# Optimization experiments

Hardware: AMD Instinct MI355X
Metric: run time of the kernel (lower is better)

The kernel has to match this reference:

```python
import jax, jax.numpy as jnp
import numpy as np

PAST = 15        # sum(num_classes[:-1])
NC = 20          # sum(num_classes)
ALPHA = 0.99
IGNORE = 255


def setup_inputs() -> dict:
    key = jax.random.key(0)
    k1, k2, k3, k4, k5, k6 = jax.random.split(key, 6)
    B, C, H, W = 8, NC, 512, 512
    logit = jax.random.normal(k1, (B, C, H, W), dtype=jnp.float32)
    # ema_prob is used as probabilities (gathered & compared to thresholds)
    ema_prob = jax.nn.softmax(jax.random.normal(k2, (B, C, H, W), dtype=jnp.float32), axis=1)
    ema_thresh = jax.random.uniform(k3, (NC,), dtype=jnp.float32, minval=0.2, maxval=0.8)
    real_labels = jax.random.randint(k4, (B, H, W), 0, NC, dtype=jnp.int64)
    # sprinkle ignore pixels (255) like real segmentation masks
    real_labels = jnp.where(jax.random.uniform(k5, (B, H, W)) < 0.1, IGNORE, real_labels)
    moving_prob_avg = jax.random.uniform(k6, (NC,), dtype=jnp.float32)
    return {"logit": logit, "ema_prob": ema_prob, "ema_thresh": ema_thresh,
            "real_labels": real_labels, "moving_prob_avg": moving_prob_avg}


def reference(logit, ema_prob, ema_thresh, real_labels, moving_prob_avg):
    # --- pseudo-labels from current model (detached softmax) ---
    logit_prob = jax.nn.softmax(jax.lax.stop_gradient(logit), axis=1)  # [B,C,H,W]
    labels = jnp.argmax(logit_prob[:, :PAST], axis=1)                   # [B,H,W]
    labels = jnp.where(real_labels >= PAST, real_labels, labels)
    idx = jnp.where(real_labels == IGNORE, 0, labels)
    scores = jnp.take_along_axis(logit_prob, idx[:, None], axis=1)[:, 0]  # [B,H,W]

    # --- per-class mean of scores + EMA update of moving_prob_avg ---
    flat_lab = labels.reshape(-1)
    flat_sc = scores.reshape(-1)
    seg = jnp.where(flat_lab == IGNORE, NC, flat_lab)  # route ignored to extra bucket
    sums = jax.ops.segment_sum(flat_sc, seg, num_segments=NC + 1)[:NC]
    counts = jax.ops.segment_sum(jnp.ones_like(flat_sc), seg, num_segments=NC + 1)[:NC]
    means = sums / jnp.maximum(counts, 1.0)
    mpa = moving_prob_avg  # numpy buffer in torch (no grad)
    new_mpa = jnp.where(counts > 0,
                        jnp.where(mpa == -1.0, means, (1.0 - ALPHA) * means + ALPHA * mpa),
                        mpa)

    # --- EMA-teacher pseudo labels + threshold mask ---
    ema_labels = jnp.argmax(ema_prob[:, :PAST], axis=1)
    ema_labels = jnp.where(real_labels >= PAST, real_labels, ema_labels)
    eidx = jnp.where(real_labels == IGNORE, 0, ema_labels)
    ema_scores = jnp.take_along_axis(ema_prob, eidx[:, None], axis=1)[:, 0]
    valid_cls = ema_labels < NC  # 255 never matches any class in the torch loop
    thr = ema_thresh[jnp.clip(ema_labels, 0, NC - 1)]
    ema_mask = valid_cls & (ema_scores >= thr)
    dynamic_labels = jnp.where(ema_mask, ema_labels, IGNORE)  # [B,H,W]

    # --- masked cross-entropy with per-class reweighting ---
    logp = jax.nn.log_softmax(logit, axis=1)
    cidx = jnp.clip(dynamic_labels, 0, NC - 1)
    losses = -jnp.take_along_axis(logp, cidx[:, None], axis=1)[:, 0]
    valid = dynamic_labels != IGNORE
    mult = jnp.where(valid, 1.0 - new_mpa[cidx], 1.0)
    losses = losses * jax.lax.stop_gradient(mult)  # multiplier is a host scalar in torch
    vs = valid.astype(losses.dtype)
    return jnp.sum(losses * vs) / jnp.sum(vs)
```

## Files before the change

kernel.cpp:

```cpp
#include <hip/hip_runtime.h>
#include <math.h>


#define PASTC 15
#define NCC   20
#define IGN   255
#define HW2   262144
#define ALPHAF 0.99f

__global__ __launch_bounds__(256) void dl_main(
    const float* __restrict__ logit,
    const float* __restrict__ ema,
    const float* __restrict__ thresh,
    const int*   __restrict__ real,
    float*       __restrict__ ws)
{
    __shared__ float s_acc[61];
    const int tid = threadIdx.x;
    if (tid < 61) s_acc[tid] = 0.0f;
    __syncthreads();

    const int t  = blockIdx.x * 256 + tid;
    const int p0 = t << 2;
    const int b  = p0 >> 18;
    const int s  = p0 & (HW2 - 1);
    const size_t base = (((size_t)(b * NCC)) << 18) + (size_t)s;

    const int4 rl4 = *reinterpret_cast<const int4*>(real + p0);
    const int rl[4] = {rl4.x, rl4.y, rl4.z, rl4.w};

    int   cap_ch[4];
    float e_m15[4], e_cap[4];
    int   e_arg[4];
#pragma unroll
    for (int j = 0; j < 4; ++j) {
        cap_ch[j] = (rl[j] == IGN) ? 0 : (rl[j] >= PASTC ? rl[j] : -1);
        e_m15[j]  = -INFINITY;
        e_cap[j]  = 0.0f;
        e_arg[j]  = 0;
    }

#pragma unroll
    for (int c = 0; c < NCC; ++c) {
        const float4 v = *reinterpret_cast<const float4*>(ema + base + ((size_t)c << 18));
        const float vv[4] = {v.x, v.y, v.z, v.w};
#pragma unroll
        for (int j = 0; j < 4; ++j) {
            if (c < PASTC && vv[j] > e_m15[j]) { e_m15[j] = vv[j]; e_arg[j] = c; }
            if (c == cap_ch[j]) e_cap[j] = vv[j];
        }
    }

    int cidx[4];
#pragma unroll
    for (int j = 0; j < 4; ++j) {
        const int   el  = (rl[j] >= PASTC) ? rl[j] : e_arg[j];
        const float esc = (cap_ch[j] >= 0) ? e_cap[j] : e_m15[j];
        const float th  = thresh[el < NCC ? el : (NCC - 1)];
        const bool  valid = (el < NCC) && (esc >= th);
        cidx[j] = valid ? el : -1;
    }

    float m20[4], se[4], m15[4], capS[4], capL[4];
    int   arg15[4];
#pragma unroll
    for (int j = 0; j < 4; ++j) {
        m20[j] = -INFINITY; se[j] = 0.0f; m15[j] = -INFINITY;
        capS[j] = 0.0f; capL[j] = 0.0f; arg15[j] = 0;
    }

#pragma unroll
    for (int c = 0; c < NCC; ++c) {
        const float4 v = *reinterpret_cast<const float4*>(logit + base + ((size_t)c << 18));
        const float vv[4] = {v.x, v.y, v.z, v.w};
#pragma unroll
        for (int j = 0; j < 4; ++j) {
            const float x  = vv[j];
            const float mo = m20[j];
            const float e  = __expf(-fabsf(x - mo));
            const bool  g  = x > mo;
            se[j]  = g ? fmaf(se[j], e, 1.0f) : (se[j] + e);
            m20[j] = fmaxf(mo, x);
            if (c < PASTC && x > m15[j]) { m15[j] = x; arg15[j] = c; }
            if (c == cap_ch[j]) capS[j] = x;
            if (c == cidx[j])   capL[j] = x;
        }
    }

#pragma unroll
    for (int j = 0; j < 4; ++j) {
        const float lse = m20[j] + __logf(se[j]);
        if (rl[j] != IGN) {
            const int   lab  = (rl[j] >= PASTC) ? rl[j] : arg15[j];
            const float sval = (cap_ch[j] >= 0) ? capS[j] : m15[j];
            const float prob = __expf(sval - lse);
            atomicAdd(&s_acc[lab], prob);
            atomicAdd(&s_acc[20 + lab], 1.0f);
        }
        if (cidx[j] >= 0) {
            atomicAdd(&s_acc[40 + cidx[j]], lse - capL[j]);
        }
        const unsigned long long bm = __ballot(cidx[j] >= 0);
        if ((tid & 63) == 0) atomicAdd(&s_acc[60], (float)__popcll(bm));
    }

    __syncthreads();
    if (tid < 61) atomicAdd(&ws[tid], s_acc[tid]);
}

__global__ void dl_final(const float* __restrict__ ws,
                         const float* __restrict__ mpa,
                         float*       __restrict__ out)
{
    if (threadIdx.x == 0 && blockIdx.x == 0) {
        float acc = 0.0f;
        for (int c = 0; c < NCC; ++c) {
            const float ssum = ws[c];
            const float cnt  = ws[20 + c];
            const float lsum = ws[40 + c];
            const float m    = mpa[c];
            const float mean = ssum / fmaxf(cnt, 1.0f);
            const float nm   = (cnt > 0.0f)
                                 ? ((m == -1.0f) ? mean
                                                 : (1.0f - ALPHAF) * mean + ALPHAF * m)
                                 : m;
            acc += lsum * (1.0f - nm);
        }
        out[0] = acc / ws[60];
    }
}

extern "C" void kernel_launch(void* const* d_in, const int* in_sizes, int n_in,
                              void* d_out, int out_size, void* d_ws, size_t ws_size,
                              hipStream_t stream) {
    const float* logit  = (const float*)d_in[0];
    const float* ema    = (const float*)d_in[1];
    const float* thresh = (const float*)d_in[2];
    const int*   real   = (const int*)d_in[3];
    const float* mpa    = (const float*)d_in[4];
    float* out = (float*)d_out;
    float* ws  = (float*)d_ws;

    hipMemsetAsync(ws, 0, 64 * sizeof(float), stream);

    dl_main<<<2048, 256, 0, stream>>>(logit, ema, thresh, real, ws);
    dl_final<<<1, 64, 0, stream>>>(ws, mpa, out);
}
```

Measured before the change: 352.8 us.

## Fuse EMA and logit passes with register prefetch and unshifted softmax sum

Merges the two per-channel loops over ema_prob and logit into a single pass. Each thread keeps a 6-deep ring of float4 registers for both tensors and issues the next channel's loads while computing the current one, so more memory requests are in flight. The logsumexp drops the running-max rescaling and just sums expf(x), which removes work but can overflow for large logits. Thresholds are staged in shared memory, and the per-wave valid-count atomics are merged into one.

```diff
diff --git a/kernel.cpp b/kernel.cpp
--- a/kernel.cpp
+++ b/kernel.cpp
@@ -7,6 +7,7 @@
 #define IGN   255
 #define HW2   262144
 #define ALPHAF 0.99f
+#define NPF   6
 
 __global__ __launch_bounds__(256) void dl_main(
     const float* __restrict__ logit,
@@ -16,8 +17,10 @@
     float*       __restrict__ ws)
 {
     __shared__ float s_acc[61];
+    __shared__ float s_thr[NCC];
     const int tid = threadIdx.x;
     if (tid < 61) s_acc[tid] = 0.0f;
+    if (tid < NCC) s_thr[tid] = thresh[tid];
     __syncthreads();
 
     const int t  = blockIdx.x * 256 + tid;
@@ -25,84 +28,84 @@
     const int b  = p0 >> 18;
     const int s  = p0 & (HW2 - 1);
     const size_t base = (((size_t)(b * NCC)) << 18) + (size_t)s;
+    const float* eb = ema   + base;
+    const float* lb = logit + base;
 
     const int4 rl4 = *reinterpret_cast<const int4*>(real + p0);
     const int rl[4] = {rl4.x, rl4.y, rl4.z, rl4.w};
 
-    int   cap_ch[4];
+    int cap_ch[4];
     float e_m15[4], e_cap[4];
-    int   e_arg[4];
+    float x_m15[4], x_cap[4];
+    float x_earg[4];
+    float se[4];
+    int   e_arg[4], arg15[4];
 #pragma unroll
     for (int j = 0; j < 4; ++j) {
         cap_ch[j] = (rl[j] == IGN) ? 0 : (rl[j] >= PASTC ? rl[j] : -1);
-        e_m15[j]  = -INFINITY;
-        e_cap[j]  = 0.0f;
-        e_arg[j]  = 0;
+        e_m15[j] = -INFINITY; x_m15[j] = -INFINITY;
+        e_cap[j] = 0.0f; x_cap[j] = 0.0f; x_earg[j] = 0.0f;
+        se[j] = 0.0f; e_arg[j] = 0; arg15[j] = 0;
+    }
+
+    float4 be[NPF], bl[NPF];
+#pragma unroll
+    for (int c = 0; c < NPF; ++c) {
+        be[c] = *reinterpret_cast<const float4*>(eb + ((size_t)c << 18));
+        bl[c] = *reinterpret_cast<const float4*>(lb + ((size_t)c << 18));
     }
 
 #pragma unroll
     for (int c = 0; c < NCC; ++c) {
-        const float4 v = *reinterpret_cast<const float4*>(ema + base + ((size_t)c << 18));
-        const float vv[4] = {v.x, v.y, v.z, v.w};
+        const int slot = c % NPF;
+        const float4 ve = be[slot];
+        const float4 vl = bl[slot];
+        if (c + NPF < NCC) {
+            be[slot] = *reinterpret_cast<const float4*>(eb + ((size_t)(c + NPF) << 18));
+            bl[slot] = *reinterpret_cast<const float4*>(lb + ((size_t)(c + NPF) << 18));
+        }
+        const float ev[4] = {ve.x, ve.y, ve.z, ve.w};
+        const float xv[4] = {vl.x, vl.y, vl.z, vl.w};
 #pragma unroll
         for (int j = 0; j < 4; ++j) {
-            if (c < PASTC && vv[j] > e_m15[j]) { e_m15[j] = vv[j]; e_arg[j] = c; }
-            if (c == cap_ch[j]) e_cap[j] = vv[j];
+            const float x  = xv[j];
+            se[j] += __expf(x);
+            if (c < PASTC) {
+                const bool gl = x > x_m15[j];
+                x_m15[j] = gl ? x : x_m15[j];
+                arg15[j] = gl ? c : arg15[j];
+                const bool ge = ev[j] > e_m15[j];
+                e_m15[j]  = ge ? ev[j] : e_m15[j];
+                e_arg[j]  = ge ? c : e_arg[j];
+                x_earg[j] = ge ? x : x_earg[j];
+            }
+            if (c == cap_ch[j]) { e_cap[j] = ev[j]; x_cap[j] = x; }
         }
     }
 
-    int cidx[4];
+    float vcnt = 0.0f;
 #pragma unroll
     for (int j = 0; j < 4; ++j) {
-        const int   el  = (rl[j] >= PASTC) ? rl[j] : e_arg[j];
-        const float esc = (cap_ch[j] >= 0) ? e_cap[j] : e_m15[j];
-        const float th  = thresh[el < NCC ? el : (NCC - 1)];
-        const bool  valid = (el < NCC) && (esc >= th);
-        cidx[j] = valid ? el : -1;
-    }
-
-    float m20[4], se[4], m15[4], capS[4], capL[4];
-    int   arg15[4];
-#pragma unroll
-    for (int j = 0; j < 4; ++j) {
-        m20[j] = -INFINITY; se[j] = 0.0f; m15[j] = -INFINITY;
-        capS[j] = 0.0f; capL[j] = 0.0f; arg15[j] = 0;
-    }
-
-#pragma unroll
-    for (int c = 0; c < NCC; ++c) {
-        const float4 v = *reinterpret_cast<const float4*>(logit + base + ((size_t)c << 18));
-        const float vv[4] = {v.x, v.y, v.z, v.w};
-#pragma unroll
-        for (int j = 0; j < 4; ++j) {
-            const float x  = vv[j];
-            const float mo = m20[j];
-            const float e  = __expf(-fabsf(x - mo));
-            const bool  g  = x > mo;
-            se[j]  = g ? fmaf(se[j], e, 1.0f) : (se[j] + e);
-            m20[j] = fmaxf(mo, x);
-            if (c < PASTC && x > m15[j]) { m15[j] = x; arg15[j] = c; }
-            if (c == cap_ch[j]) capS[j] = x;
-            if (c == cidx[j])   capL[j] = x;
-        }
-    }
-
-#pragma unroll
-    for (int j = 0; j < 4; ++j) {
-        const float lse = m20[j] + __logf(se[j]);
+        const float lse = __logf(se[j]);
         if (rl[j] != IGN) {
             const int   lab  = (rl[j] >= PASTC) ? rl[j] : arg15[j];
-            const float sval = (cap_ch[j] >= 0) ? capS[j] : m15[j];
-            const float prob = __expf(sval - lse);
+            const float xsc  = (cap_ch[j] >= 0) ? x_cap[j] : x_m15[j];
+            const float prob = __expf(xsc - lse);
             atomicAdd(&s_acc[lab], prob);
             atomicAdd(&s_acc[20 + lab], 1.0f);
         }
-        if (cidx[j] >= 0) {
-            atomicAdd(&s_acc[40 + cidx[j]], lse - capL[j]);
+        const int   el  = (rl[j] >= PASTC) ? rl[j] : e_arg[j];
+        const float esc = (rl[j] >= PASTC) ? e_cap[j] : e_m15[j];
+        const float th  = s_thr[el < NCC ? el : (NCC - 1)];
+        const bool  valid = (el < NCC) && (esc >= th);
+        if (valid) {
+            const float xel = (rl[j] >= PASTC) ? x_cap[j] : x_earg[j];
+            atomicAdd(&s_acc[40 + el], lse - xel);
         }
-        const unsigned long long bm = __ballot(cidx[j] >= 0);
-        if ((tid & 63) == 0) atomicAdd(&s_acc[60], (float)__popcll(bm));
+        const unsigned long long bm = __ballot(valid);
+        if ((tid & 63) == 0) vcnt += (float)__popcll(bm);
     }
+    if ((tid & 63) == 0) atomicAdd(&s_acc[60], vcnt);
 
     __syncthreads();
     if (tid < 61) atomicAdd(&ws[tid], s_acc[tid]);
```

Measured after the change: 346.4 us. Within noise of the previous version (-1.8%).
